# Kernel tuning notes

Hardware: AMD Instinct MI355X
Metric: run time of the kernel (lower is better)

The kernel has to match this reference:

```python
import jax, jax.numpy as jnp
import numpy as np

B, S, HID, NH, HD = 2, 2048, 1024, 16, 64
SCALE = 1.0 / np.sqrt(HD)
NEG = -1e9


def _rope_cache(seq_len, dim, base=10000.0):
    inv_freq = 1.0 / (base ** (np.arange(0, dim, 2, dtype=np.float32) / dim))
    t = np.arange(seq_len, dtype=np.float32)
    freqs = np.outer(t, inv_freq)                      # [S, dim/2]
    emb = np.concatenate([freqs, freqs], axis=-1)      # [S, dim]
    return jnp.asarray(np.cos(emb)), jnp.asarray(np.sin(emb))


def _rotate_half(x):
    x1, x2 = jnp.split(x, 2, axis=-1)
    return jnp.concatenate([-x2, x1], axis=-1)


def setup_inputs() -> dict:
    key = jax.random.key(0)
    k0, k1, k2, k3, k4 = jax.random.split(key, 5)
    hidden_states = jax.random.normal(k0, (B, S, HID), jnp.float32)
    Wq = jax.random.normal(k1, (HID, NH * HD), jnp.float32) * 0.02
    Wk = jax.random.normal(k2, (HID, NH * HD), jnp.float32) * 0.02
    Wv = jax.random.normal(k3, (HID, NH * HD), jnp.float32) * 0.02
    Wo = jax.random.normal(k4, (NH * HD, HID), jnp.float32) * 0.02
    causal = jnp.tril(jnp.ones((S, S), bool))
    attention_mask = jnp.broadcast_to(
        jnp.where(causal, 0.0, NEG).astype(jnp.float32)[None, None], (B, 1, S, S))
    position_ids = jnp.broadcast_to(jnp.arange(S, dtype=jnp.int32)[None], (B, S))
    cos, sin = _rope_cache(S, HD)
    return {"hidden_states": hidden_states, "attention_mask": attention_mask,
            "position_ids": position_ids, "cos": cos, "sin": sin,
            "Wq": Wq, "Wk": Wk, "Wv": Wv, "Wo": Wo}


def reference(hidden_states, attention_mask, position_ids, cos, sin, Wq, Wk, Wv, Wo):
    b, s, _ = hidden_states.shape
    def proj(W):  # [B,S,HID] @ [HID,NH*HD] -> [B,NH,S,HD]
        return jnp.einsum('bsh,hd->bsd', hidden_states, W).reshape(b, s, NH, HD).transpose(0, 2, 1, 3)
    q, k, v = proj(Wq), proj(Wk), proj(Wv)
    # RoPE: gather per-position cos/sin -> [B,1,S,HD]
    cos_g = cos[position_ids][:, None]
    sin_g = sin[position_ids][:, None]
    q = q * cos_g + _rotate_half(q) * sin_g
    k = k * cos_g + _rotate_half(k) * sin_g
    scores = jnp.einsum('bhqd,bhkd->bhqk', q, k) * SCALE + attention_mask
    attn = jax.nn.softmax(scores.astype(jnp.float32), axis=-1).astype(q.dtype)
    out = jnp.einsum('bhqk,bhkd->bhqd', attn, v)
    out = out.transpose(0, 2, 1, 3).reshape(b, s, NH * HD)
    return jnp.einsum('bsd,dh->bsh', out, Wo)
```

## Files before the change

### kernel.cpp

```cpp
#include <hip/hip_runtime.h>

typedef __bf16 bf16x8 __attribute__((ext_vector_type(8)));
typedef float  f32x4  __attribute__((ext_vector_type(4)));
typedef unsigned short ushortx8 __attribute__((ext_vector_type(8)));
typedef unsigned short ushortx4 __attribute__((ext_vector_type(4)));

static __device__ __forceinline__ unsigned short f2bf(float f) {
  unsigned int u = __builtin_bit_cast(unsigned int, f);
  u += 0x7FFFu + ((u >> 16) & 1u);
  return (unsigned short)(u >> 16);
}
static __device__ __forceinline__ unsigned short f2bf_fast(float f) {
  unsigned int u = __builtin_bit_cast(unsigned int, f);
  return (unsigned short)((u + 0x8000u) >> 16);
}

#define GLL16(gp, lp) __builtin_amdgcn_global_load_lds(                       \
    (const __attribute__((address_space(1))) void*)(gp),                      \
    (__attribute__((address_space(3))) void*)(lp), 16, 0, 0)

__global__ __launch_bounds__(256) void prep_kernel(const float* __restrict__ X,
                                                   const float* __restrict__ W0,
                                                   const float* __restrict__ W1,
                                                   const float* __restrict__ W2,
                                                   const float* __restrict__ W3,
                                                   unsigned short* __restrict__ Xbf,
                                                   unsigned short* __restrict__ D0,
                                                   unsigned short* __restrict__ D1,
                                                   unsigned short* __restrict__ D2,
                                                   unsigned short* __restrict__ D3) {
  int z = blockIdx.z;
  if (z >= 4) {
    long bid = (long)(z - 4) * 1024 + blockIdx.y * 32 + blockIdx.x;
    int tl = threadIdx.y * 32 + threadIdx.x;
    long i = bid * 2048 + (long)tl * 8;
    float4 f0 = *(const float4*)(X + i);
    float4 f1 = *(const float4*)(X + i + 4);
    ushortx8 u;
    u[0] = f2bf(f0.x); u[1] = f2bf(f0.y); u[2] = f2bf(f0.z); u[3] = f2bf(f0.w);
    u[4] = f2bf(f1.x); u[5] = f2bf(f1.y); u[6] = f2bf(f1.z); u[7] = f2bf(f1.w);
    *(ushortx8*)(Xbf + i) = u;
    return;
  }
  const float* src = (z == 0) ? W0 : (z == 1) ? W1 : (z == 2) ? W2 : W3;
  unsigned short* dst = (z == 0) ? D0 : (z == 1) ? D1 : (z == 2) ? D2 : D3;
  const int R = 1024, C = 1024;
  __shared__ unsigned short t[32][33];
  int c = blockIdx.x * 32 + threadIdx.x;
#pragma unroll
  for (int i = 0; i < 4; ++i) {
    int r = blockIdx.y * 32 + threadIdx.y + i * 8;
    t[threadIdx.y + i * 8][threadIdx.x] = f2bf(src[(size_t)r * C + c]);
  }
  __syncthreads();
  int rr = blockIdx.y * 32 + threadIdx.x;
#pragma unroll
  for (int i = 0; i < 4; ++i) {
    int cc = blockIdx.x * 32 + threadIdx.y + i * 8;
    dst[(size_t)cc * R + rr] = t[threadIdx.x][threadIdx.y + i * 8];
  }
}

__global__ __launch_bounds__(256) void gemm128_kernel(
    const unsigned short* __restrict__ A,
    const unsigned short* __restrict__ BT0,
    const unsigned short* __restrict__ BT1,
    const unsigned short* __restrict__ BT2,
    unsigned short* __restrict__ outQ,
    unsigned short* __restrict__ outK,
    unsigned short* __restrict__ outVT,
    const int* __restrict__ pos_ids,
    const float* __restrict__ cosb,
    const float* __restrict__ sinb) {
  const int K = 1024;
  int id = blockIdx.x + 8 * (blockIdx.y + 32 * blockIdx.z);
  int m_idx = id & 31;
  int nzi = id >> 5;
  int n_idx = nzi & 7;
  int z = nzi >> 3;
  const unsigned short* BT = (z == 0) ? BT0 : (z == 1 ? BT1 : BT2);
  int n0 = n_idx * 128, m0 = m_idx * 128;
  int t = threadIdx.x, lane = t & 63, w = t >> 6;
  int wy = w >> 1, wx = w & 1;
  int n16 = lane & 15, quad = lane >> 4;
  __shared__ __align__(16) unsigned short sA0[128 * 32];
  __shared__ __align__(16) unsigned short sA1[128 * 32];
  __shared__ __align__(16) unsigned short sB0[128 * 32];
  __shared__ __align__(16) unsigned short sB1[128 * 32];

  int r4 = lane >> 2, c4 = lane & 3;
  const char* gA = (const char*)(A + (size_t)(m0 + w * 32 + r4) * K) + ((c4 ^ (r4 & 3)) * 16);
  const char* gB = (const char*)(BT + (size_t)(n0 + w * 32 + r4) * K) + ((c4 ^ (r4 & 3)) * 16);
  const size_t row16 = (size_t)16 * K * 2;

  f32x4 acc[4][4];
#pragma unroll
  for (int i = 0; i < 4; ++i)
#pragma unroll
    for (int j = 0; j < 4; ++j) acc[i][j] = f32x4{0.f, 0.f, 0.f, 0.f};

#define GSTAGE(kk_, SA, SB)                                                     \
  do {                                                                          \
    GLL16(gA + (size_t)(kk_) * 2, SA + (w * 32) * 32);                          \
    GLL16(gA + (size_t)(kk_) * 2 + row16, SA + (w * 32 + 16) * 32);             \
    GLL16(gB + (size_t)(kk_) * 2, SB + (w * 32) * 32);                          \
    GLL16(gB + (size_t)(kk_) * 2 + row16, SB + (w * 32 + 16) * 32);             \
  } while (0)

#define GCOMPUTE(SA, SB)                                                        \
  do {                                                                          \
    bf16x8 a[4], b[4];                                                          \
    int cs = (quad ^ (n16 & 3)) * 8;                                            \
    _Pragma("unroll") for (int i = 0; i < 4; ++i) {                             \
      a[i] = *(const bf16x8*)(&SA[(wy * 64 + i * 16 + n16) * 32 + cs]);         \
      b[i] = *(const bf16x8*)(&SB[(wx * 64 + i * 16 + n16) * 32 + cs]);         \
    }                                                                           \
    _Pragma("unroll") for (int mt = 0; mt < 4; ++mt)                            \
      _Pragma("unroll") for (int nt = 0; nt < 4; ++nt)                          \
        acc[mt][nt] = __builtin_amdgcn_mfma_f32_16x16x32_bf16(                  \
            a[mt], b[nt], acc[mt][nt], 0, 0, 0);                                \
  } while (0)

  GSTAGE(0, sA0, sB0);
  for (int kk = 0; kk < K;) {
    __syncthreads();
    if (kk + 32 < K) GSTAGE(kk + 32, sA1, sB1);
    GCOMPUTE(sA0, sB0);
    kk += 32;
    if (kk >= K) break;
    __syncthreads();
    if (kk + 32 < K) GSTAGE(kk + 32, sA0, sB0);
    GCOMPUTE(sA1, sB1);
    kk += 32;
  }
#undef GSTAGE
#undef GCOMPUTE

  if (z < 2) {
    const float qs = (z == 0) ? (0.125f * 1.44269504088896340736f) : 1.0f;
#pragma unroll
    for (int mt = 0; mt < 4; ++mt)
#pragma unroll
      for (int r = 0; r < 4; ++r) {
        int row = m0 + wy * 64 + mt * 16 + quad * 4 + r;
        int b = row >> 11, s = row & 2047;
        int pos = pos_ids[b * 2048 + s];
        const float* cb = cosb + (size_t)pos * 64;
        const float* sb = sinb + (size_t)pos * 64;
#pragma unroll
        for (int nt = 0; nt < 2; ++nt) {
          int d0 = nt * 16 + n16;
          float c0 = cb[d0] * qs, s0 = sb[d0] * qs;
          float c1 = cb[d0 + 32] * qs, s1 = sb[d0 + 32] * qs;
          float x0 = acc[mt][nt][r], x1 = acc[mt][nt + 2][r];
          acc[mt][nt][r]     = x0 * c0 - x1 * s0;
          acc[mt][nt + 2][r] = x1 * c1 + x0 * s1;
        }
      }
  }

  if (z == 2) {
#pragma unroll
    for (int mt = 0; mt < 4; ++mt)
#pragma unroll
      for (int nt = 0; nt < 4; ++nt) {
        int row = m0 + wy * 64 + mt * 16 + quad * 4;
        int b = row >> 11, s = row & 2047;
        int col = n0 + wx * 64 + nt * 16 + n16;
        int h = col >> 6, d = col & 63;
        ushortx4 u;
#pragma unroll
        for (int r = 0; r < 4; ++r) u[r] = f2bf(acc[mt][nt][r]);
        *(ushortx4*)(&outVT[(((size_t)b * 16 + h) * 64 + d) * 2048 + s]) = u;
      }
    return;
  }

#pragma unroll
  for (int mt = 0; mt < 4; ++mt)
#pragma unroll
    for (int nt = 0; nt < 4; ++nt)
#pragma unroll
      for (int r = 0; r < 4; ++r) {
        int row = m0 + wy * 64 + mt * 16 + quad * 4 + r;
        int col = n0 + wx * 64 + nt * 16 + n16;
        unsigned short* dst = (z == 0) ? outQ : outK;
        int b = row >> 11, s = row & 2047, h = col >> 6, d = col & 63;
        dst[(((size_t)b * 16 + h) * 2048 + s) * 64 + d] = f2bf(acc[mt][nt][r]);
      }
}

__global__ __launch_bounds__(256) void gemm64_kernel(const unsigned short* __restrict__ A,
                                                     const unsigned short* __restrict__ BT,
                                                     float* __restrict__ outF) {
  const int K = 1024, N = 1024;
  int m0 = blockIdx.x * 64, n0 = blockIdx.y * 64;
  int t = threadIdx.x, lane = t & 63, w = t >> 6;
  int wy = w >> 1, wx = w & 1;
  int n16 = lane & 15, quad = lane >> 4;
  __shared__ __align__(16) unsigned short sA0[64 * 32];
  __shared__ __align__(16) unsigned short sA1[64 * 32];
  __shared__ __align__(16) unsigned short sB0[64 * 32];
  __shared__ __align__(16) unsigned short sB1[64 * 32];

  int r4 = lane >> 2, c4 = lane & 3;
  const char* gA = (const char*)(A + (size_t)(m0 + w * 16 + r4) * K) + ((c4 ^ (r4 & 3)) * 16);
  const char* gB = (const char*)(BT + (size_t)(n0 + w * 16 + r4) * K) + ((c4 ^ (r4 & 3)) * 16);

  f32x4 acc[2][2];
#pragma unroll
  for (int i = 0; i < 2; ++i)
#pragma unroll
    for (int j = 0; j < 2; ++j) acc[i][j] = f32x4{0.f, 0.f, 0.f, 0.f};

#define WSTAGE(kk_, SA, SB)                                                     \
  do {                                                                          \
    GLL16(gA + (size_t)(kk_) * 2, SA + (w * 16) * 32);                          \
    GLL16(gB + (size_t)(kk_) * 2, SB + (w * 16) * 32);                          \
  } while (0)

#define WCOMPUTE(SA, SB)                                                        \
  do {                                                                          \
    int cs = (quad ^ (n16 & 3)) * 8;                                            \
    bf16x8 a0 = *(const bf16x8*)(&SA[(wy * 32 + n16) * 32 + cs]);               \
    bf16x8 a1 = *(const bf16x8*)(&SA[(wy * 32 + 16 + n16) * 32 + cs]);          \
    bf16x8 b0 = *(const bf16x8*)(&SB[(wx * 32 + n16) * 32 + cs]);               \
    bf16x8 b1 = *(const bf16x8*)(&SB[(wx * 32 + 16 + n16) * 32 + cs]);          \
    acc[0][0] = __builtin_amdgcn_mfma_f32_16x16x32_bf16(a0, b0, acc[0][0], 0, 0, 0); \
    acc[0][1] = __builtin_amdgcn_mfma_f32_16x16x32_bf16(a0, b1, acc[0][1], 0, 0, 0); \
    acc[1][0] = __builtin_amdgcn_mfma_f32_16x16x32_bf16(a1, b0, acc[1][0], 0, 0, 0); \
    acc[1][1] = __builtin_amdgcn_mfma_f32_16x16x32_bf16(a1, b1, acc[1][1], 0, 0, 0); \
  } while (0)

  WSTAGE(0, sA0, sB0);
  for (int kk = 0; kk < K;) {
    __syncthreads();
    if (kk + 32 < K) WSTAGE(kk + 32, sA1, sB1);
    WCOMPUTE(sA0, sB0);
    kk += 32;
    if (kk >= K) break;
    __syncthreads();
    if (kk + 32 < K) WSTAGE(kk + 32, sA0, sB0);
    WCOMPUTE(sA1, sB1);
    kk += 32;
  }
#undef WSTAGE
#undef WCOMPUTE

#pragma unroll
  for (int mt = 0; mt < 2; ++mt)
#pragma unroll
    for (int nt = 0; nt < 2; ++nt)
#pragma unroll
      for (int r = 0; r < 4; ++r) {
        int row = m0 + wy * 32 + mt * 16 + quad * 4 + r;
        int col = n0 + wx * 32 + nt * 16 + n16;
        outF[(size_t)row * N + col] = acc[mt][nt][r];
      }
}

__global__ __launch_bounds__(512) void attn_kernel(const unsigned short* __restrict__ Q,
                                                   const unsigned short* __restrict__ Kk,
                                                   const unsigned short* __restrict__ VT,
                                                   unsigned short* __restrict__ O) {
  int bh = blockIdx.x;
  int qt = (int)(gridDim.y - 1 - blockIdx.y);
  int t = threadIdx.x;
  int lane = t & 63;
  int w = t >> 6;
  int g = w >> 2;
  int w4 = w & 3;
  int n16 = lane & 15, quad = lane >> 4;
  int r8 = lane >> 3, c8 = lane & 7;
  const unsigned short* Qb = Q + (size_t)bh * 2048 * 64;
  const unsigned short* Kb = Kk + (size_t)bh * 2048 * 64;
  const unsigned short* Vb = VT + (size_t)bh * 64 * 2048;

  __shared__ __align__(16) unsigned short sKV[2 * 2 * 2 * 4096];
  __shared__ __align__(16) unsigned short sP[8][16 * 64];
  unsigned short* spW = sP[w];
  unsigned short* gBase = sKV + g * 16384;

  int b_ = bh >> 4, h_ = bh & 15;
  int nk = qt + 1;
  int u = (nk + 1) >> 1;
  int beg = g ? u : 0;
  int end = g ? nk : u;
  int qg = qt * 64 + w4 * 16 + n16;

  bf16x8 aQ[2];
#pragma unroll
  for (int kb = 0; kb < 2; ++kb)
    aQ[kb] = *(const bf16x8*)(Qb + (size_t)qg * 64 + kb * 32 + quad * 8);

  f32x4 o[4];
  float mst = -3e38f, lst = 0.f;
#pragma unroll
  for (int ct = 0; ct < 4; ++ct) o[ct] = f32x4{0.f, 0.f, 0.f, 0.f};

#define ASTAGE(kt_, BUF)                                                                  \
  do {                                                                                    \
    const unsigned short* kg_ = Kb + (size_t)((kt_) * 64 + w4 * 16) * 64;                 \
    const unsigned short* vg_ = Vb + (size_t)(w4 * 16) * 2048 + (kt_) * 64;               \
    unsigned short* dK = gBase + (BUF) * 8192 + (w4 * 16) * 64;                           \
    unsigned short* dV = dK + 4096;                                                       \
    GLL16(kg_ + (size_t)r8 * 64 + (c8 ^ r8) * 8, dK);                                     \
    GLL16(kg_ + (size_t)(8 + r8) * 64 + (c8 ^ r8) * 8, dK + 8 * 64);                      \
    GLL16(vg_ + (size_t)r8 * 2048 + (c8 ^ r8) * 8, dV);                                   \
    GLL16(vg_ + (size_t)(8 + r8) * 2048 + (c8 ^ r8) * 8, dV + 8 * 64);                    \
  } while (0)

#define ACOMPUTE(kt_, BUF)                                                                \
  do {                                                                                    \
    const unsigned short* kT_ = gBase + (BUF) * 8192;                                     \
    const unsigned short* vT_ = kT_ + 4096;                                               \
    f32x4 sc[4];                                \
    _Pragma("unroll") for (int mt = 0; mt < 4; ++mt) {                                    \
      const unsigned short* kr = &kT_[(mt * 16 + n16) * 64];                              \
      bf16x8 ka0 = *(const bf16x8*)(kr + ((quad ^ (n16 & 7)) * 8));                       \
      bf16x8 ka1 = *(const bf16x8*)(kr + (((4 + quad) ^ (n16 & 7)) * 8));                 \
      f32x4 zv = f32x4{0.f, 0.f, 0.f, 0.f};                                               \
      zv = __builtin_amdgcn_mfma_f32_16x16x32_bf16(ka0, aQ[0], zv, 0, 0, 0);              \
      sc[mt] = __builtin_amdgcn_mfma_f32_16x16x32_bf16(ka1, aQ[1], zv, 0, 0, 0);          \
    }                                                                                     \
    float p[4][4];                                                                        \
    _Pragma("unroll") for (int mt = 0; mt < 4; ++mt)                                      \
      _Pragma("unroll") for (int r = 0; r < 4; ++r) p[mt][r] = sc[mt][r];                 \
    if ((kt_) == nk - 1) {                                 \
      int kb0 = (kt_) * 64 + quad * 4;                                                    \
      _Pragma("unroll") for (int mt = 0; mt < 4; ++mt)                                    \
        _Pragma("unroll") for (int r = 0; r < 4; ++r)                                     \
          if (kb0 + mt * 16 + r > qg) p[mt][r] = -3e38f;                                  \
    }                                                                                     \
    float rm = p[0][0];                                                                   \
    _Pragma("unroll") for (int mt = 0; mt < 4; ++mt)                                      \
      _Pragma("unroll") for (int r = 0; r < 4; ++r) rm = fmaxf(rm, p[mt][r]);             \
    rm = fmaxf(rm, __shfl_xor(rm, 16));                                                   \
    rm = fmaxf(rm, __shfl_xor(rm, 32));                                                   \
    float mn = fmaxf(mst, rm);                                                            \
    float al = exp2f(mst - mn);                                                           \
    mst = mn;                                                                             \
    float rs = 0.f;                                                                       \
    _Pragma("unroll") for (int mt = 0; mt < 4; ++mt)                                      \
      _Pragma("unroll") for (int r = 0; r < 4; ++r) {                                     \
        p[mt][r] = exp2f(p[mt][r] - mn);                                                  \
        rs += p[mt][r];                                                                   \
      }                                                                                   \
    lst = lst * al + rs;                                                                  \
    _Pragma("unroll") for (int ct = 0; ct < 4; ++ct)                                      \
      _Pragma("unroll") for (int r = 0; r < 4; ++r) o[ct][r] *= al;                       \
    _Pragma("unroll") for (int mt = 0; mt < 4; ++mt) {                                    \
      ushortx4 uu;                                                                        \
      _Pragma("unroll") for (int r = 0; r < 4; ++r) uu[r] = f2bf_fast(p[mt][r]);          \
      int ch = (mt * 2 + (quad >> 1)) ^ (n16 & 7);                                        \
      *(ushortx4*)(&spW[n16 * 64 + ch * 8 + (quad & 1) * 4]) = uu;                        \
    }                                                                                     \
    __builtin_amdgcn_s_waitcnt(0xC07F);     \
    bf16x8 aP0 = *(const bf16x8*)(&spW[n16 * 64 + ((quad ^ (n16 & 7)) * 8)]);             \
    bf16x8 aP1 = *(const bf16x8*)(&spW[n16 * 64 + (((4 + quad) ^ (n16 & 7)) * 8)]);       \
    _Pragma("unroll") for (int ct = 0; ct < 4; ++ct) {                                    \
      const unsigned short* vr = &vT_[(ct * 16 + n16) * 64];                              \
      bf16x8 va0 = *(const bf16x8*)(vr + ((quad ^ (n16 & 7)) * 8));                       \
      bf16x8 va1 = *(const bf16x8*)(vr + (((4 + quad) ^ (n16 & 7)) * 8));                 \
      o[ct] = __builtin_amdgcn_mfma_f32_16x16x32_bf16(va0, aP0, o[ct], 0, 0, 0);          \
      o[ct] = __builtin_amdgcn_mfma_f32_16x16x32_bf16(va1, aP1, o[ct], 0, 0, 0);          \
    }                                                                                     \
  } while (0)

  if (beg < end) ASTAGE(beg, 0);
  int it = 0;
  while (it < u) {
    __syncthreads();
    {
      int kt = beg + it;
      if (kt + 1 < end) ASTAGE(kt + 1, 1);
      if (kt < end) ACOMPUTE(kt, 0);
    }
    if (++it >= u) break;
    __syncthreads();
    {
      int kt = beg + it;
      if (kt + 1 < end) ASTAGE(kt + 1, 0);
      if (kt < end) ACOMPUTE(kt, 1);
    }
    ++it;
  }
#undef ASTAGE
#undef ACOMPUTE

  lst += __shfl_xor(lst, 16);
  lst += __shfl_xor(lst, 32);

  __syncthreads();
  float* scratch = (float*)sKV;
  int sidx = (w4 * 64 + lane) * 18;
  if (g == 1) {
#pragma unroll
    for (int ct = 0; ct < 4; ++ct)
#pragma unroll
      for (int r = 0; r < 4; ++r) scratch[sidx + ct * 4 + r] = o[ct][r];
    scratch[sidx + 16] = mst;
    scratch[sidx + 17] = lst;
  }
  __syncthreads();
  if (g == 0) {
    float m1 = scratch[sidx + 16], l1 = scratch[sidx + 17];
    float m = fmaxf(mst, m1);
    float a0 = exp2f(mst - m), a1 = exp2f(m1 - m);
    float inv = 1.0f / (lst * a0 + l1 * a1);
#pragma unroll
    for (int ct = 0; ct < 4; ++ct) {
      ushortx4 uo;
#pragma unroll
      for (int r = 0; r < 4; ++r) {
        float v = (o[ct][r] * a0 + scratch[sidx + ct * 4 + r] * a1) * inv;
        uo[r] = f2bf(v);
      }
      size_t addr = ((size_t)b_ * 2048 + qg) * 1024 + h_ * 64 + ct * 16 + quad * 4;
      *(ushortx4*)(&O[addr]) = uo;
    }
  }
}

extern "C" void kernel_launch(void* const* d_in, const int* in_sizes, int n_in,
                              void* d_out, int out_size, void* d_ws, size_t ws_size,
                              hipStream_t stream) {
  const float* X    = (const float*)d_in[0];
  const int*   pos  = (const int*)d_in[2];
  const float* cosb = (const float*)d_in[3];
  const float* sinb = (const float*)d_in[4];
  const float* Wq   = (const float*)d_in[5];
  const float* Wk   = (const float*)d_in[6];
  const float* Wv   = (const float*)d_in[7];
  const float* Wo   = (const float*)d_in[8];
  float* out = (float*)d_out;

  char* ws = (char*)d_ws;
  const size_t SZ_X = 4096UL * 1024 * 2;
  const size_t SZ_W = 1024UL * 1024 * 2;
  unsigned short* Xbf = (unsigned short*)(ws);
  unsigned short* WTq = (unsigned short*)(ws + SZ_X);
  unsigned short* WTk = (unsigned short*)(ws + SZ_X + SZ_W);
  unsigned short* WTv = (unsigned short*)(ws + SZ_X + 2 * SZ_W);
  unsigned short* WTo = (unsigned short*)(ws + SZ_X + 3 * SZ_W);
  unsigned short* Qbf = (unsigned short*)(ws + SZ_X + 4 * SZ_W);
  unsigned short* Kbf = (unsigned short*)(ws + 2 * SZ_X + 4 * SZ_W);
  unsigned short* VTr = (unsigned short*)(ws + 3 * SZ_X + 4 * SZ_W);
  unsigned short* Obf = (unsigned short*)(ws + 4 * SZ_X + 4 * SZ_W);

  prep_kernel<<<dim3(32, 32, 6), dim3(32, 8), 0, stream>>>(
      X, Wq, Wk, Wv, Wo, Xbf, WTq, WTk, WTv, WTo);

  gemm128_kernel<<<dim3(8, 32, 3), 256, 0, stream>>>(Xbf, WTq, WTk, WTv,
                                                     Qbf, Kbf, VTr,
                                                     pos, cosb, sinb);

  attn_kernel<<<dim3(32, 32), 512, 0, stream>>>(Qbf, Kbf, VTr, Obf);

  gemm64_kernel<<<dim3(64, 16), 256, 0, stream>>>(Obf, WTo, out);
}
```

Baseline: 209.9 us.

## Rewrite QKV projection GEMM with 256x256 tiles and a barrier-interleaved MFMA pipeline

The QKV projection GEMM moves from 128x128 tiles with 256 threads to 256x256 tiles with 512 threads (8 waves, 128x64 per wave). It uses a double-buffered K=64 stage split into two 32-wide halves, and interleaves global-to-LDS loads, LDS reads and MFMA quadrants between explicit barriers, raising s_setprio around the MFMA blocks. The aim is more data reuse per tile and better overlap of memory and compute. In exchange the grid shrinks to 192 workgroups, which may underfill the GPU, and register and LDS pressure rise.

```diff
diff --git a/kernel.cpp b/kernel.cpp
--- a/kernel.cpp
+++ b/kernel.cpp
@@ -61,7 +61,7 @@
   }
 }
 
-__global__ __launch_bounds__(256) void gemm128_kernel(
+__global__ __launch_bounds__(512, 2) void gemm256_kernel(
     const unsigned short* __restrict__ A,
     const unsigned short* __restrict__ BT0,
     const unsigned short* __restrict__ BT1,
@@ -73,121 +73,175 @@
     const float* __restrict__ cosb,
     const float* __restrict__ sinb) {
   const int K = 1024;
-  int id = blockIdx.x + 8 * (blockIdx.y + 32 * blockIdx.z);
-  int m_idx = id & 31;
-  int nzi = id >> 5;
-  int n_idx = nzi & 7;
-  int z = nzi >> 3;
+  int id = blockIdx.x * 24 + blockIdx.y;
+  int z = id >> 6;
+  int r_ = id & 63;
+  int n_idx = r_ & 3, m_idx = r_ >> 2;
   const unsigned short* BT = (z == 0) ? BT0 : (z == 1 ? BT1 : BT2);
-  int n0 = n_idx * 128, m0 = m_idx * 128;
+  int m0 = m_idx * 256, n0 = n_idx * 256;
   int t = threadIdx.x, lane = t & 63, w = t >> 6;
-  int wy = w >> 1, wx = w & 1;
+  int wy = w >> 2, wx = w & 3;
   int n16 = lane & 15, quad = lane >> 4;
-  __shared__ __align__(16) unsigned short sA0[128 * 32];
-  __shared__ __align__(16) unsigned short sA1[128 * 32];
-  __shared__ __align__(16) unsigned short sB0[128 * 32];
-  __shared__ __align__(16) unsigned short sB1[128 * 32];
-
-  int r4 = lane >> 2, c4 = lane & 3;
-  const char* gA = (const char*)(A + (size_t)(m0 + w * 32 + r4) * K) + ((c4 ^ (r4 & 3)) * 16);
-  const char* gB = (const char*)(BT + (size_t)(n0 + w * 32 + r4) * K) + ((c4 ^ (r4 & 3)) * 16);
-  const size_t row16 = (size_t)16 * K * 2;
-
-  f32x4 acc[4][4];
-#pragma unroll
-  for (int i = 0; i < 4; ++i)
+
+  __shared__ __align__(16) unsigned short sA[2][2][256][32];
+  __shared__ __align__(16) unsigned short sB[2][2][256][32];
+
+  const char* gA0 = (const char*)(A + (size_t)(m0 + (w & 3) * 16 + (lane >> 2)) * K
+                                  + (w >> 2) * 32 + ((lane & 3) ^ ((lane >> 2) & 3)) * 8);
+  const char* gB0 = (const char*)(BT + (size_t)(n0 + (w & 3) * 16 + (lane >> 2)) * K
+                                  + (w >> 2) * 32 + ((lane & 3) ^ ((lane >> 2) & 3)) * 8);
+  unsigned short* ldsA_w = &sA[0][w >> 2][(w & 3) * 16][0];
+  unsigned short* ldsB_w = &sB[0][w >> 2][(w & 3) * 16][0];
+
+  const unsigned short* rdA = &sA[0][0][wy * 128 + n16][(quad ^ (n16 & 3)) * 8];
+  const unsigned short* rdB = &sB[0][0][wx * 64 + n16][(quad ^ (n16 & 3)) * 8];
+
+  f32x4 acc[8][4];
+#pragma unroll
+  for (int i = 0; i < 8; ++i)
 #pragma unroll
     for (int j = 0; j < 4; ++j) acc[i][j] = f32x4{0.f, 0.f, 0.f, 0.f};
 
-#define GSTAGE(kk_, SA, SB)                                                     \
-  do {                                                                          \
-    GLL16(gA + (size_t)(kk_) * 2, SA + (w * 32) * 32);                          \
-    GLL16(gA + (size_t)(kk_) * 2 + row16, SA + (w * 32 + 16) * 32);             \
-    GLL16(gB + (size_t)(kk_) * 2, SB + (w * 32) * 32);                          \
-    GLL16(gB + (size_t)(kk_) * 2 + row16, SB + (w * 32 + 16) * 32);             \
-  } while (0)
-
-#define GCOMPUTE(SA, SB)                                                        \
-  do {                                                                          \
-    bf16x8 a[4], b[4];                                                          \
-    int cs = (quad ^ (n16 & 3)) * 8;                                            \
-    _Pragma("unroll") for (int i = 0; i < 4; ++i) {                             \
-      a[i] = *(const bf16x8*)(&SA[(wy * 64 + i * 16 + n16) * 32 + cs]);         \
-      b[i] = *(const bf16x8*)(&SB[(wx * 64 + i * 16 + n16) * 32 + cs]);         \
-    }                                                                           \
-    _Pragma("unroll") for (int mt = 0; mt < 4; ++mt)                            \
-      _Pragma("unroll") for (int nt = 0; nt < 4; ++nt)                          \
-        acc[mt][nt] = __builtin_amdgcn_mfma_f32_16x16x32_bf16(                  \
-            a[mt], b[nt], acc[mt][nt], 0, 0, 0);                                \
-  } while (0)
-
-  GSTAGE(0, sA0, sB0);
-  for (int kk = 0; kk < K;) {
-    __syncthreads();
-    if (kk + 32 < K) GSTAGE(kk + 32, sA1, sB1);
-    GCOMPUTE(sA0, sB0);
-    kk += 32;
-    if (kk >= K) break;
-    __syncthreads();
-    if (kk + 32 < K) GSTAGE(kk + 32, sA0, sB0);
-    GCOMPUTE(sA1, sB1);
-    kk += 32;
-  }
-#undef GSTAGE
-#undef GCOMPUTE
+  bf16x8 a[4][2], b[2][2];
+
+#define STG_A(db, kt, H)                                                              \
+  do {                                                                                \
+    GLL16(gA0 + (size_t)((H) * 128) * 2048 + (kt) * 128,                              \
+          ldsA_w + (db) * 16384 + ((H) * 128) * 32);                                  \
+    GLL16(gA0 + (size_t)((H) * 128 + 64) * 2048 + (kt) * 128,                         \
+          ldsA_w + (db) * 16384 + ((H) * 128 + 64) * 32);                             \
+  } while (0)
+#define STG_B(db, kt, H)                                                              \
+  do {                                                                                \
+    GLL16(gB0 + (size_t)((H) * 128) * 2048 + (kt) * 128,                              \
+          ldsB_w + (db) * 16384 + ((H) * 128) * 32);                                  \
+    GLL16(gB0 + (size_t)((H) * 128 + 64) * 2048 + (kt) * 128,                         \
+          ldsB_w + (db) * 16384 + ((H) * 128 + 64) * 32);                             \
+  } while (0)
+
+#define RD_A(db, mh)                                                                  \
+  do {                                                                                \
+    _Pragma("unroll") for (int i = 0; i < 4; ++i) {                                   \
+      a[i][0] = *(const bf16x8*)(rdA + (db) * 16384 + ((mh) * 64 + i * 16) * 32);     \
+      a[i][1] = *(const bf16x8*)(rdA + (db) * 16384 + 8192 + ((mh) * 64 + i * 16) * 32); \
+    }                                                                                 \
+  } while (0)
+#define RD_B(db, nh)                                                                  \
+  do {                                                                                \
+    _Pragma("unroll") for (int jj = 0; jj < 2; ++jj) {                                \
+      b[jj][0] = *(const bf16x8*)(rdB + (db) * 16384 + ((nh) * 32 + jj * 16) * 32);   \
+      b[jj][1] = *(const bf16x8*)(rdB + (db) * 16384 + 8192 + ((nh) * 32 + jj * 16) * 32); \
+    }                                                                                 \
+  } while (0)
+
+#define MM(mh, nh)                                                                    \
+  do {                                                                                \
+    _Pragma("unroll") for (int i = 0; i < 4; ++i)                                     \
+      _Pragma("unroll") for (int jj = 0; jj < 2; ++jj) {                              \
+        acc[(mh) * 4 + i][(nh) * 2 + jj] = __builtin_amdgcn_mfma_f32_16x16x32_bf16(   \
+            a[i][0], b[jj][0], acc[(mh) * 4 + i][(nh) * 2 + jj], 0, 0, 0);            \
+        acc[(mh) * 4 + i][(nh) * 2 + jj] = __builtin_amdgcn_mfma_f32_16x16x32_bf16(   \
+            a[i][1], b[jj][1], acc[(mh) * 4 + i][(nh) * 2 + jj], 0, 0, 0);            \
+      }                                                                               \
+  } while (0)
+
+#define BARRIER_MFMA(mh, nh, VM)                                                      \
+  do {                                                                                \
+    if (VM) asm volatile("s_waitcnt vmcnt(0)" ::: "memory");                          \
+    __builtin_amdgcn_s_barrier();                                                     \
+    asm volatile("s_waitcnt lgkmcnt(0)" ::: "memory");                                \
+    __builtin_amdgcn_sched_barrier(0);                                                \
+    __builtin_amdgcn_s_setprio(1);                                                    \
+    MM(mh, nh);                                                                       \
+    __builtin_amdgcn_s_setprio(0);                                                    \
+    __builtin_amdgcn_sched_barrier(0);                                                \
+    __builtin_amdgcn_s_barrier();                                                     \
+  } while (0)
+
+  STG_A(0, 0, 0); STG_A(0, 0, 1); STG_B(0, 0, 0); STG_B(0, 0, 1);
+  asm volatile("s_waitcnt vmcnt(0)" ::: "memory");
+  __builtin_amdgcn_s_barrier();
+
+  for (int j = 0; j < 8; ++j) {
+    int t1 = 2 * j + 1, t2 = 2 * j + 2;
+    bool more = (j < 7);
+    RD_A(0, 0); RD_B(0, 0);
+    STG_A(1, t1, 0); STG_A(1, t1, 1);
+    BARRIER_MFMA(0, 0, 0);
+    RD_B(0, 1);
+    STG_B(1, t1, 0); STG_B(1, t1, 1);
+    BARRIER_MFMA(0, 1, 0);
+    RD_A(0, 1);
+    BARRIER_MFMA(1, 1, 0);
+    RD_B(0, 0);
+    BARRIER_MFMA(1, 0, 1);
+    RD_A(1, 0); RD_B(1, 0);
+    if (more) { STG_A(0, t2, 0); STG_A(0, t2, 1); }
+    BARRIER_MFMA(0, 0, 0);
+    RD_B(1, 1);
+    if (more) { STG_B(0, t2, 0); STG_B(0, t2, 1); }
+    BARRIER_MFMA(0, 1, 0);
+    RD_A(1, 1);
+    BARRIER_MFMA(1, 1, 0);
+    RD_B(1, 0);
+    BARRIER_MFMA(1, 0, 1);
+  }
+#undef STG_A
+#undef STG_B
+#undef RD_A
+#undef RD_B
+#undef MM
+#undef BARRIER_MFMA
 
   if (z < 2) {
     const float qs = (z == 0) ? (0.125f * 1.44269504088896340736f) : 1.0f;
 #pragma unroll
-    for (int mt = 0; mt < 4; ++mt)
+    for (int mi = 0; mi < 8; ++mi)
 #pragma unroll
       for (int r = 0; r < 4; ++r) {
-        int row = m0 + wy * 64 + mt * 16 + quad * 4 + r;
-        int b = row >> 11, s = row & 2047;
-        int pos = pos_ids[b * 2048 + s];
+        int row = m0 + wy * 128 + mi * 16 + quad * 4 + r;
+        int b_ = row >> 11, s_ = row & 2047;
+        int pos = pos_ids[b_ * 2048 + s_];
         const float* cb = cosb + (size_t)pos * 64;
         const float* sb = sinb + (size_t)pos * 64;
 #pragma unroll
-        for (int nt = 0; nt < 2; ++nt) {
-          int d0 = nt * 16 + n16;
+        for (int ni = 0; ni < 2; ++ni) {
+          int d0 = ni * 16 + n16;
           float c0 = cb[d0] * qs, s0 = sb[d0] * qs;
           float c1 = cb[d0 + 32] * qs, s1 = sb[d0 + 32] * qs;
-          float x0 = acc[mt][nt][r], x1 = acc[mt][nt + 2][r];
-          acc[mt][nt][r]     = x0 * c0 - x1 * s0;
-          acc[mt][nt + 2][r] = x1 * c1 + x0 * s1;
+          float x0 = acc[mi][ni][r], x1 = acc[mi][ni + 2][r];
+          acc[mi][ni][r]     = x0 * c0 - x1 * s0;
+          acc[mi][ni + 2][r] = x1 * c1 + x0 * s1;
         }
       }
-  }
-
-  if (z == 2) {
-#pragma unroll
-    for (int mt = 0; mt < 4; ++mt)
-#pragma unroll
-      for (int nt = 0; nt < 4; ++nt) {
-        int row = m0 + wy * 64 + mt * 16 + quad * 4;
-        int b = row >> 11, s = row & 2047;
-        int col = n0 + wx * 64 + nt * 16 + n16;
-        int h = col >> 6, d = col & 63;
-        ushortx4 u;
-#pragma unroll
-        for (int r = 0; r < 4; ++r) u[r] = f2bf(acc[mt][nt][r]);
-        *(ushortx4*)(&outVT[(((size_t)b * 16 + h) * 64 + d) * 2048 + s]) = u;
-      }
+    unsigned short* dst = (z == 0) ? outQ : outK;
+#pragma unroll
+    for (int mi = 0; mi < 8; ++mi)
+#pragma unroll
+      for (int ni = 0; ni < 4; ++ni)
+#pragma unroll
+        for (int r = 0; r < 4; ++r) {
+          int row = m0 + wy * 128 + mi * 16 + quad * 4 + r;
+          int col = n0 + wx * 64 + ni * 16 + n16;
+          int b_ = row >> 11, s_ = row & 2047, h_ = col >> 6, d_ = col & 63;
+          dst[(((size_t)b_ * 16 + h_) * 2048 + s_) * 64 + d_] = f2bf(acc[mi][ni][r]);
+        }
     return;
   }
 
 #pragma unroll
-  for (int mt = 0; mt < 4; ++mt)
-#pragma unroll
-    for (int nt = 0; nt < 4; ++nt)
-#pragma unroll
-      for (int r = 0; r < 4; ++r) {
-        int row = m0 + wy * 64 + mt * 16 + quad * 4 + r;
-        int col = n0 + wx * 64 + nt * 16 + n16;
-        unsigned short* dst = (z == 0) ? outQ : outK;
-        int b = row >> 11, s = row & 2047, h = col >> 6, d = col & 63;
-        dst[(((size_t)b * 16 + h) * 2048 + s) * 64 + d] = f2bf(acc[mt][nt][r]);
-      }
+  for (int mi = 0; mi < 8; ++mi)
+#pragma unroll
+    for (int ni = 0; ni < 4; ++ni) {
+      int row = m0 + wy * 128 + mi * 16 + quad * 4;
+      int b_ = row >> 11, s_ = row & 2047;
+      int col = n0 + wx * 64 + ni * 16 + n16;
+      int h_ = col >> 6, d_ = col & 63;
+      ushortx4 u;
+#pragma unroll
+      for (int r = 0; r < 4; ++r) u[r] = f2bf(acc[mi][ni][r]);
+      *(ushortx4*)(&outVT[(((size_t)b_ * 16 + h_) * 64 + d_) * 2048 + s_]) = u;
+    }
 }
 
 __global__ __launch_bounds__(256) void gemm64_kernel(const unsigned short* __restrict__ A,
@@ -451,9 +505,9 @@
   prep_kernel<<<dim3(32, 32, 6), dim3(32, 8), 0, stream>>>(
       X, Wq, Wk, Wv, Wo, Xbf, WTq, WTk, WTv, WTo);
 
-  gemm128_kernel<<<dim3(8, 32, 3), 256, 0, stream>>>(Xbf, WTq, WTk, WTv,
-                                                     Qbf, Kbf, VTr,
-                                                     pos, cosb, sinb);
+  gemm256_kernel<<<dim3(8, 24), 512, 0, stream>>>(Xbf, WTq, WTk, WTv,
+                                                  Qbf, Kbf, VTr,
+                                                  pos, cosb, sinb);
 
   attn_kernel<<<dim3(32, 32), 512, 0, stream>>>(Qbf, Kbf, VTr, Obf);
 
```

New measurement: 209.9 us. Within noise of the previous version (-0.0%).
